# Kernel tuning notes

Hardware: AMD Instinct MI355X
Metric: run time of the kernel (lower is better)

Reference implementation:

```python
import jax, jax.numpy as jnp
import numpy as np

D = 1024      # n_embd
H = 16        # n_head
HD = D // H   # head_size = 64


def _layernorm(x, g, b, eps=1e-5):
    mu = jnp.mean(x, axis=-1, keepdims=True)
    var = jnp.mean((x - mu) ** 2, axis=-1, keepdims=True)
    return (x - mu) * jax.lax.rsqrt(var + eps) * g + b


def setup_inputs() -> dict:
    key = jax.random.key(0)
    ks = jax.random.split(key, 12)
    s = lambda fan_in: 1.0 / np.sqrt(fan_in)
    inp = {
        "x": jax.random.normal(ks[0], (4, 2048, D), dtype=jnp.float32),
        # attention projections (bias=False in Head), per-head weights fused into [D, D]
        "wq": jax.random.uniform(ks[1], (D, D), jnp.float32, -s(D), s(D)),
        "wk": jax.random.uniform(ks[2], (D, D), jnp.float32, -s(D), s(D)),
        "wv": jax.random.uniform(ks[3], (D, D), jnp.float32, -s(D), s(D)),
        "wo": jax.random.uniform(ks[4], (D, D), jnp.float32, -s(D), s(D)),
        "bo": jax.random.uniform(ks[5], (D,), jnp.float32, -s(D), s(D)),
        # feed-forward: D -> 4D -> D
        "w1": jax.random.uniform(ks[6], (D, 4 * D), jnp.float32, -s(D), s(D)),
        "b1": jax.random.uniform(ks[7], (4 * D,), jnp.float32, -s(D), s(D)),
        "w2": jax.random.uniform(ks[8], (4 * D, D), jnp.float32, -s(4 * D), s(4 * D)),
        "b2": jax.random.uniform(ks[9], (D,), jnp.float32, -s(4 * D), s(4 * D)),
        # layernorms
        "g_ln1": jnp.ones((D,), jnp.float32),
        "b_ln1": jnp.zeros((D,), jnp.float32),
        "g_ln2": jnp.ones((D,), jnp.float32),
        "b_ln2": jnp.zeros((D,), jnp.float32),
    }
    return inp


def reference(x, wq, wk, wv, wo, bo, w1, b1, w2, b2, g_ln1, b_ln1, g_ln2, b_ln2):
    B, T, _ = x.shape
    # --- self-attention on ln1(x) ---
    h = _layernorm(x, g_ln1, b_ln1)
    q = (h @ wq).reshape(B, T, H, HD)
    k = (h @ wk).reshape(B, T, H, HD)
    v = (h @ wv).reshape(B, T, H, HD)
    scores = jnp.einsum("bqhd,bkhd->bhqk", q, k) * (HD ** -0.5)
    causal = jnp.tril(jnp.ones((T, T), dtype=bool))
    scores = jnp.where(causal, scores, -jnp.inf)
    wei = jax.nn.softmax(scores, axis=-1)                    # [B,H,T,T]
    attn = jnp.einsum("bhqk,bkhd->bqhd", wei, v).reshape(B, T, D)
    x = x + attn @ wo + bo
    # --- feed-forward on ln2(x) ---
    h2 = _layernorm(x, g_ln2, b_ln2)
    x = x + jax.nn.relu(h2 @ w1 + b1) @ w2 + b2
    return x
```

## Files before the change

kernel.cpp:

```cpp
#include <hip/hip_runtime.h>
#include <cstdint>

typedef __bf16 bf16x8 __attribute__((ext_vector_type(8)));
typedef float f32x4 __attribute__((ext_vector_type(4)));
typedef unsigned int u32x4 __attribute__((ext_vector_type(4)));
typedef unsigned int u32x2 __attribute__((ext_vector_type(2)));
typedef unsigned short u16x4 __attribute__((ext_vector_type(4)));

#define D_MODEL 1024
#define SEQ     2048
#define NBATCH  4
#define NHEAD   16
#define HDIM    64
#define NTOK    (NBATCH * SEQ)
#define QSCALE  0.18033688011112042f

__device__ __forceinline__ unsigned short f2bf(float f) {
  unsigned int u = __builtin_bit_cast(unsigned int, f);
  u += 0x7FFFu + ((u >> 16) & 1u);
  return (unsigned short)(u >> 16);
}

__device__ __forceinline__ float bf2f(unsigned short s) {
  return __builtin_bit_cast(float, (unsigned int)s << 16);
}

__device__ __forceinline__ bf16x8 load8bf(const unsigned short* p) {
  return __builtin_bit_cast(bf16x8, *(const u32x4*)p);
}

__device__ __forceinline__ f32x4 mfma16(bf16x8 a, bf16x8 b, f32x4 c) {
  return __builtin_amdgcn_mfma_f32_16x16x32_bf16(a, b, c, 0, 0, 0);
}

__device__ __forceinline__ void gload16(const unsigned short* g, unsigned short* l) {
  __builtin_amdgcn_global_load_lds((__attribute__((address_space(1))) void*)g,
                                   (__attribute__((address_space(3))) void*)l, 16, 0, 0);
}

__global__ __launch_bounds__(256) void tcast_all(const float* __restrict__ wq,
                                                 const float* __restrict__ wk,
                                                 const float* __restrict__ wv,
                                                 const float* __restrict__ wo,
                                                 const float* __restrict__ w1,
                                                 const float* __restrict__ w2,
                                                 unsigned short* __restrict__ wqkv_t,
                                                 unsigned short* __restrict__ wo_t,
                                                 unsigned short* __restrict__ w1_t,
                                                 unsigned short* __restrict__ w2_t) {
  const int id = blockIdx.x;
  const float* in; unsigned short* out; int K, N, k0, n0;
  if (id < 4096) {
    const int seg = id >> 10, r = id & 1023;
    in  = seg == 0 ? wq : seg == 1 ? wk : seg == 2 ? wv : wo;
    out = seg == 3 ? wo_t : wqkv_t + (size_t)seg * 1024 * 1024;
    K = 1024; N = 1024; n0 = (r & 31) * 32; k0 = (r >> 5) * 32;
  } else if (id < 8192) {
    const int r = id - 4096;
    in = w1; out = w1_t; K = 1024; N = 4096;
    n0 = (r & 127) * 32; k0 = (r >> 7) * 32;
  } else {
    const int r = id - 8192;
    in = w2; out = w2_t; K = 4096; N = 1024;
    n0 = (r & 31) * 32; k0 = (r >> 5) * 32;
  }
  __shared__ float tile[32][33];
  const int tx = threadIdx.x & 31, ty = threadIdx.x >> 5;
  #pragma unroll
  for (int j = 0; j < 4; ++j)
    tile[ty + 8 * j][tx] = in[(size_t)(k0 + ty + 8 * j) * N + n0 + tx];
  __syncthreads();
  #pragma unroll
  for (int j = 0; j < 4; ++j)
    out[(size_t)(n0 + ty + 8 * j) * K + k0 + tx] = f2bf(tile[tx][ty + 8 * j]);
}

template <int FPIN>
__global__ __launch_bounds__(256) void ln_kernel(const void* __restrict__ xin,
                                                 const float* __restrict__ g,
                                                 const float* __restrict__ bb,
                                                 unsigned short* __restrict__ out) {
  const int row = blockIdx.x, tid = threadIdx.x;
  float4 xv;
  if (FPIN) {
    xv = ((const float4*)((const float*)xin + (size_t)row * D_MODEL))[tid];
  } else {
    const u16x4 bv4 = ((const u16x4*)((const unsigned short*)xin + (size_t)row * D_MODEL))[tid];
    xv.x = bf2f(bv4.x); xv.y = bf2f(bv4.y); xv.z = bf2f(bv4.z); xv.w = bf2f(bv4.w);
  }
  float s  = xv.x + xv.y + xv.z + xv.w;
  float ss = xv.x * xv.x + xv.y * xv.y + xv.z * xv.z + xv.w * xv.w;
  #pragma unroll
  for (int off = 1; off < 64; off <<= 1) { s += __shfl_xor(s, off); ss += __shfl_xor(ss, off); }
  __shared__ float red[8];
  const int wave = tid >> 6, lane = tid & 63;
  if (lane == 0) { red[wave] = s; red[4 + wave] = ss; }
  __syncthreads();
  s  = red[0] + red[1] + red[2] + red[3];
  ss = red[4] + red[5] + red[6] + red[7];
  const float mu   = s * (1.0f / D_MODEL);
  const float var  = ss * (1.0f / D_MODEL) - mu * mu;
  const float rstd = rsqrtf(var + 1e-5f);
  const float4 gv = ((const float4*)g)[tid];
  const float4 bv = ((const float4*)bb)[tid];
  u16x4 o;
  o.x = f2bf((xv.x - mu) * rstd * gv.x + bv.x);
  o.y = f2bf((xv.y - mu) * rstd * gv.y + bv.y);
  o.z = f2bf((xv.z - mu) * rstd * gv.z + bv.z);
  o.w = f2bf((xv.w - mu) * rstd * gv.w + bv.w);
  *(u16x4*)(out + (size_t)row * D_MODEL + tid * 4) = o;
}

template <bool BIAS, bool RELU, int RES, bool OBF>
__global__ __launch_bounds__(256) void gemm_bt(const unsigned short* __restrict__ A,
                                               const unsigned short* __restrict__ Bt,
                                               const float* __restrict__ bias,
                                               const void* __restrict__ res,
                                               void* __restrict__ out,
                                               int M, int N, int K) {
  __shared__ __align__(16) unsigned short As[128 * 64];
  __shared__ __align__(16) unsigned short Bs[128 * 64];
  const int tid  = threadIdx.x;
  const int lin = blockIdx.y * gridDim.x + blockIdx.x;
  const int xcd = lin & 7, idx = lin >> 3;
  const int by = xcd * 8 + (idx & 7);
  const int bx = idx >> 3;
  const int row0 = by * 128, col0 = bx * 128;
  const int wave = tid >> 6, lane = tid & 63;
  const int wm = wave >> 1, wn = wave & 1;
  const int l15 = lane & 15, quad = lane >> 4;
  f32x4 acc[4][4] = {};

  const int tr = tid >> 3;
  const int tc = (tid & 7) ^ (tr & 7);
  const unsigned short* gA = A  + (size_t)(row0 + tr) * K + tc * 8;
  const unsigned short* gB = Bt + (size_t)(col0 + tr) * K + tc * 8;

  const int rowA = (wm * 64 + l15) * 64;
  const int rowB = (wn * 64 + l15) * 64;
  const int swz0 = (quad ^ (l15 & 7)) * 8;
  const int swz1 = ((4 + quad) ^ (l15 & 7)) * 8;

  for (int k0 = 0; k0 < K; k0 += 64) {
    #pragma unroll
    for (int i = 0; i < 4; ++i) {
      gload16(gA + (size_t)(i * 32) * K + k0, As + (i * 256 + tid) * 8);
      gload16(gB + (size_t)(i * 32) * K + k0, Bs + (i * 256 + tid) * 8);
    }
    __syncthreads();
    #pragma unroll
    for (int kf = 0; kf < 2; ++kf) {
      const int swz = kf ? swz1 : swz0;
      bf16x8 af[4], bfr[4];
      #pragma unroll
      for (int t = 0; t < 4; ++t) {
        af[t]  = load8bf(As + rowA + t * 1024 + swz);
        bfr[t] = load8bf(Bs + rowB + t * 1024 + swz);
      }
      #pragma unroll
      for (int i = 0; i < 4; ++i)
        #pragma unroll
        for (int j = 0; j < 4; ++j)
          acc[i][j] = mfma16(af[i], bfr[j], acc[i][j]);
    }
    __syncthreads();
  }

  const size_t rbase = (size_t)row0 + wm * 64 + quad * 4;
  const int cbase = col0 + wn * 64 + l15;
  #pragma unroll
  for (int i = 0; i < 4; ++i) {
    #pragma unroll
    for (int j = 0; j < 4; ++j) {
      const int col = cbase + j * 16;
      const float bval = BIAS ? bias[col] : 0.0f;
      #pragma unroll
      for (int r = 0; r < 4; ++r) {
        const size_t row = rbase + i * 16 + r;
        float v = acc[i][j][r];
        if (BIAS) v += bval;
        if (RELU) v = fmaxf(v, 0.0f);
        if (RES == 1) v += ((const float*)res)[row * N + col];
        if (RES == 2) v += bf2f(((const unsigned short*)res)[row * N + col]);
        if (OBF)  ((unsigned short*)out)[row * N + col] = f2bf(v);
        else      ((float*)out)[row * N + col] = v;
      }
    }
  }
}

__device__ __forceinline__ void stage_half_512(const unsigned short* __restrict__ src,
                                               unsigned short* dst, int ld, int k0,
                                               int h, int tid) {
  #pragma unroll
  for (int l = 0; l < 2; ++l) {
    const int cid = l * 512 + tid;
    const int r = cid >> 3, p = cid & 7, c = p ^ (r & 7);
    gload16(src + (size_t)(h * 128 + r) * ld + k0 + c * 8, dst + h * 8192 + cid * 8);
  }
}

template <bool BIAS, bool RELU, int RES, bool OBF, bool QKV>
__global__ __launch_bounds__(512, 2) void gemm256(const unsigned short* __restrict__ A,
                                                  const unsigned short* __restrict__ Bt,
                                                  const float* __restrict__ bias,
                                                  const void* __restrict__ res,
                                                  void* __restrict__ out,
                                                  unsigned short* __restrict__ qb,
                                                  unsigned short* __restrict__ kp,
                                                  unsigned short* __restrict__ vt,
                                                  int M, int N, int K) {
  __shared__ __align__(16) unsigned short lds[2][32768];
  const int tid = threadIdx.x;
  const int lin = blockIdx.y * gridDim.x + blockIdx.x;
  const int xcd = lin & 7, idx = lin >> 3;
  const int by = xcd * 4 + (idx & 3);
  const int bx = idx >> 2;
  const int row0 = by * 256, col0 = bx * 256;
  const int wave = tid >> 6, lane = tid & 63;
  const int wm = wave >> 2, wn = wave & 3;
  const int l15 = lane & 15, quad = lane >> 4;
  const int swz0 = (quad ^ (l15 & 7)) * 8;
  const int swz1 = ((4 + quad) ^ (l15 & 7)) * 8;

  const unsigned short* gA = A  + (size_t)row0 * K;
  const unsigned short* gB = Bt + (size_t)col0 * K;

  unsigned short* As0 = &lds[0][0];
  unsigned short* Bs0 = &lds[0][16384];
  unsigned short* As1 = &lds[1][0];
  unsigned short* Bs1 = &lds[1][16384];

  f32x4 acc[8][4] = {};
  const int KT = K >> 6;

  stage_half_512(gA, As0, K, 0, 0, tid);
  stage_half_512(gA, As0, K, 0, 1, tid);
  stage_half_512(gB, Bs0, K, 0, 0, tid);
  stage_half_512(gB, Bs0, K, 0, 1, tid);
  if (KT > 1) {
    stage_half_512(gB, Bs1, K, 64, 0, tid);
    stage_half_512(gB, Bs1, K, 64, 1, tid);
    asm volatile("s_waitcnt vmcnt(4)" ::: "memory");
  } else {
    asm volatile("s_waitcnt vmcnt(0)" ::: "memory");
  }
  asm volatile("s_barrier" ::: "memory");

  for (int t = 0; t < KT; ++t) {
    unsigned short* As  = (t & 1) ? As1 : As0;
    unsigned short* Bs  = (t & 1) ? Bs1 : Bs0;
    unsigned short* Asn = (t & 1) ? As0 : As1;
    const int k1 = (t + 1) << 6, k2 = (t + 2) << 6;
    bf16x8 a0[2][4], b01[2][2], b23[2][2];

    #pragma unroll
    for (int i = 0; i < 4; ++i) {
      const unsigned short* ap = As + (wm * 128 + i * 16 + l15) * 64;
      a0[0][i] = load8bf(ap + swz0);
      a0[1][i] = load8bf(ap + swz1);
    }
    #pragma unroll
    for (int j = 0; j < 2; ++j) {
      const unsigned short* bp = Bs + (wn * 64 + j * 16 + l15) * 64;
      b01[0][j] = load8bf(bp + swz0);
      b01[1][j] = load8bf(bp + swz1);
      const unsigned short* bp2 = Bs + (wn * 64 + 32 + j * 16 + l15) * 64;
      b23[0][j] = load8bf(bp2 + swz0);
      b23[1][j] = load8bf(bp2 + swz1);
    }
    if (t + 1 < KT) {
      stage_half_512(gA, Asn, K, k1, 0, tid);
      stage_half_512(gA, Asn, K, k1, 1, tid);
    }
    __builtin_amdgcn_s_setprio(1);
    #pragma unroll
    for (int kf = 0; kf < 2; ++kf)
      #pragma unroll
      for (int i = 0; i < 4; ++i)
        #pragma unroll
        for (int j = 0; j < 2; ++j)
          acc[i][j] = mfma16(a0[kf][i], b01[kf][j], acc[i][j]);
    #pragma unroll
    for (int kf = 0; kf < 2; ++kf)
      #pragma unroll
      for (int i = 0; i < 4; ++i)
        #pragma unroll
        for (int j = 0; j < 2; ++j)
          acc[i][2 + j] = mfma16(a0[kf][i], b23[kf][j], acc[i][2 + j]);
    __builtin_amdgcn_s_setprio(0);
    __builtin_amdgcn_sched_barrier(0);
    asm volatile("s_barrier" ::: "memory");

    #pragma unroll
    for (int i = 0; i < 4; ++i) {
      const unsigned short* ap = As + (wm * 128 + 64 + i * 16 + l15) * 64;
      a0[0][i] = load8bf(ap + swz0);
      a0[1][i] = load8bf(ap + swz1);
    }
    if (t + 2 < KT) {
      stage_half_512(gB, Bs, K, k2, 0, tid);
      stage_half_512(gB, Bs, K, k2, 1, tid);
    }
    __builtin_amdgcn_s_setprio(1);
    #pragma unroll
    for (int kf = 0; kf < 2; ++kf)
      #pragma unroll
      for (int i = 0; i < 4; ++i)
        #pragma unroll
        for (int j = 0; j < 2; ++j)
          acc[4 + i][2 + j] = mfma16(a0[kf][i], b23[kf][j], acc[4 + i][2 + j]);
    #pragma unroll
    for (int kf = 0; kf < 2; ++kf)
      #pragma unroll
      for (int i = 0; i < 4; ++i)
        #pragma unroll
        for (int j = 0; j < 2; ++j)
          acc[4 + i][j] = mfma16(a0[kf][i], b01[kf][j], acc[4 + i][j]);
    __builtin_amdgcn_s_setprio(0);
    __builtin_amdgcn_sched_barrier(0);
    if (t + 2 < KT) asm volatile("s_waitcnt vmcnt(4)" ::: "memory");
    else            asm volatile("s_waitcnt vmcnt(0)" ::: "memory");
    asm volatile("s_barrier" ::: "memory");
  }

  const size_t rbase = (size_t)row0 + wm * 128 + quad * 4;
  const int cbase = col0 + wn * 64 + l15;
  if (QKV) {
    const int sec = col0 >> 10;
    #pragma unroll
    for (int i = 0; i < 8; ++i) {
      #pragma unroll
      for (int j = 0; j < 4; ++j) {
        const int col = cbase + j * 16;
        if (sec == 0) {
          #pragma unroll
          for (int r = 0; r < 4; ++r) {
            const size_t row = rbase + i * 16 + r;
            qb[row * 1024 + col] = f2bf(acc[i][j][r] * QSCALE);
          }
        } else if (sec == 1) {
          const int c2 = col - 1024, hh = c2 >> 6, d = c2 & 63;
          #pragma unroll
          for (int r = 0; r < 4; ++r) {
            const size_t row = rbase + i * 16 + r;
            const int bb = (int)(row >> 11), tt = (int)(row & 2047);
            kp[(((size_t)(bb * 16 + hh)) * SEQ + tt) * 64 + d] = f2bf(acc[i][j][r]);
          }
        } else {
          const int c2 = col - 2048, hh = c2 >> 6, d = c2 & 63;
          const size_t t0 = rbase + i * 16;
          const int bb = (int)(t0 >> 11);
          u16x4 pk;
          #pragma unroll
          for (int r = 0; r < 4; ++r) pk[r] = f2bf(acc[i][j][r]);
          *(u16x4*)(vt + ((size_t)(bb * 16 + hh) * 64 + d) * SEQ + (t0 & 2047)) = pk;
        }
      }
    }
  } else {
    #pragma unroll
    for (int i = 0; i < 8; ++i) {
      #pragma unroll
      for (int j = 0; j < 4; ++j) {
        const int col = cbase + j * 16;
        const float bval = BIAS ? bias[col] : 0.0f;
        #pragma unroll
        for (int r = 0; r < 4; ++r) {
          const size_t row = rbase + i * 16 + r;
          float v = acc[i][j][r];
          if (BIAS) v += bval;
          if (RELU) v = fmaxf(v, 0.0f);
          if (RES == 1) v += ((const float*)res)[row * N + col];
          if (RES == 2) v += bf2f(((const unsigned short*)res)[row * N + col]);
          if (OBF)  ((unsigned short*)out)[row * N + col] = f2bf(v);
          else      ((float*)out)[row * N + col] = v;
        }
      }
    }
  }
  (void)M;
}

__device__ __forceinline__ void stage32g(const unsigned short* __restrict__ src,
                                         unsigned short* dst, int ld, int k0,
                                         int h128, int t256) {
  #pragma unroll
  for (int l = 0; l < 2; ++l) {
    const int cid = l * 256 + t256;
    const int L = cid >> 3;
    const int p = cid & 7;
    const int c = p ^ (L & 7);
    const int row = h128 * 128 + L * 2 + (c >> 2);
    gload16(src + (size_t)row * ld + k0 + (c & 3) * 8, dst + h128 * 4096 + cid * 8);
  }
}

__device__ __forceinline__ bf16x8 frag32(const unsigned short* tile, int r0,
                                         int l15, int quad) {
  const int row = r0 + l15;
  const int L = row >> 1;
  const int p = ((row & 1) * 4 + quad) ^ (L & 7);
  return load8bf(tile + L * 64 + p * 8);
}

__global__ __launch_bounds__(512, 2) void gemm_ffn2(const unsigned short* __restrict__ A,
                                                    const unsigned short* __restrict__ Bt,
                                                    const float* __restrict__ bias,
                                                    const unsigned short* __restrict__ res,
                                                    float* __restrict__ out) {
  __shared__ __align__(16) unsigned short lds[2][2][12288];
  const int tid = threadIdx.x;
  const int lin = blockIdx.y * gridDim.x + blockIdx.x;
  const int xcd = lin & 7, idx = lin >> 3;
  const int by = xcd * 4 + (idx & 3);
  const int bx = idx >> 2;
  const int row0 = by * 256, col0 = bx * 128;
  const int wave = tid >> 6, lane = tid & 63;
  const int ks = wave >> 2;
  const int w4 = wave & 3;
  const int wm = w4 >> 1, wn = w4 & 1;
  const int l15 = lane & 15, quad = lane >> 4;
  const int t256 = tid & 255;

  const unsigned short* gA = A  + (size_t)row0 * 4096 + ks * 2048;
  const unsigned short* gB = Bt + (size_t)col0 * 4096 + ks * 2048;

  unsigned short* As0 = &lds[ks][0][0];
  unsigned short* Bs0 = &lds[ks][0][8192];
  unsigned short* As1 = &lds[ks][1][0];
  unsigned short* Bs1 = &lds[ks][1][8192];

  f32x4 acc[8][4] = {};
  const int KT = 64;

  stage32g(gA, As0, 4096, 0, 0, t256);
  stage32g(gA, As0, 4096, 0, 1, t256);
  stage32g(gB, Bs0, 4096, 0, 0, t256);
  stage32g(gB, Bs1, 4096, 32, 0, t256);
  asm volatile("s_waitcnt vmcnt(2)" ::: "memory");
  asm volatile("s_barrier" ::: "memory");

  for (int t = 0; t < KT; ++t) {
    unsigned short* As  = (t & 1) ? As1 : As0;
    unsigned short* Bs  = (t & 1) ? Bs1 : Bs0;
    unsigned short* Asn = (t & 1) ? As0 : As1;
    const int k1 = (t + 1) << 5, k2 = (t + 2) << 5;
    bf16x8 a[4], b[4];

    #pragma unroll
    for (int j = 0; j < 4; ++j) b[j] = frag32(Bs, wn * 64 + j * 16, l15, quad);
    #pragma unroll
    for (int i = 0; i < 4; ++i) a[i] = frag32(As, wm * 128 + i * 16, l15, quad);
    if (t + 1 < KT) {
      stage32g(gA, Asn, 4096, k1, 0, t256);
      stage32g(gA, Asn, 4096, k1, 1, t256);
    }
    __builtin_amdgcn_s_setprio(1);
    #pragma unroll
    for (int i = 0; i < 4; ++i)
      #pragma unroll
      for (int j = 0; j < 4; ++j)
        acc[i][j] = mfma16(a[i], b[j], acc[i][j]);
    __builtin_amdgcn_s_setprio(0);
    __builtin_amdgcn_sched_barrier(0);
    asm volatile("s_barrier" ::: "memory");

    #pragma unroll
    for (int i = 0; i < 4; ++i) a[i] = frag32(As, wm * 128 + 64 + i * 16, l15, quad);
    if (t + 2 < KT) stage32g(gB, Bs, 4096, k2, 0, t256);
    __builtin_amdgcn_s_setprio(1);
    #pragma unroll
    for (int i = 0; i < 4; ++i)
      #pragma unroll
      for (int j = 0; j < 4; ++j)
        acc[4 + i][j] = mfma16(a[i], b[j], acc[4 + i][j]);
    __builtin_amdgcn_s_setprio(0);
    __builtin_amdgcn_sched_barrier(0);
    if (t + 2 < KT) asm volatile("s_waitcnt vmcnt(2)" ::: "memory");
    else            asm volatile("s_waitcnt vmcnt(0)" ::: "memory");
    asm volatile("s_barrier" ::: "memory");
  }

  float* ex = (float*)&lds[0][0][0];
  #pragma unroll
  for (int half = 0; half < 2; ++half) {
    __syncthreads();
    if (ks == 1) {
      #pragma unroll
      for (int i = 0; i < 4; ++i)
        #pragma unroll
        for (int j = 0; j < 4; ++j)
          *(f32x4*)(ex + ((size_t)(w4 * 16 + i * 4 + j)) * 256 + lane * 4) =
              acc[half * 4 + i][j];
    }
    __syncthreads();
    if (ks == 0) {
      #pragma unroll
      for (int i = 0; i < 4; ++i)
        #pragma unroll
        for (int j = 0; j < 4; ++j) {
          const f32x4 v = *(const f32x4*)(ex + ((size_t)(w4 * 16 + i * 4 + j)) * 256 + lane * 4);
          acc[half * 4 + i][j] += v;
        }
    }
  }
  if (ks == 0) {
    const size_t rbase = (size_t)row0 + wm * 128 + quad * 4;
    const int cbase = col0 + wn * 64 + l15;
    #pragma unroll
    for (int i = 0; i < 8; ++i) {
      #pragma unroll
      for (int j = 0; j < 4; ++j) {
        const int col = cbase + j * 16;
        const float bval = bias[col];
        #pragma unroll
        for (int r = 0; r < 4; ++r) {
          const size_t row = rbase + i * 16 + r;
          out[row * 1024 + col] = acc[i][j][r] + bval + bf2f(res[row * 1024 + col]);
        }
      }
    }
  }
}

__global__ __launch_bounds__(256) void attn5(const unsigned short* __restrict__ qb,
                                             const unsigned short* __restrict__ kp,
                                             const unsigned short* __restrict__ vt,
                                             unsigned short* __restrict__ attnb) {
  const int lin = (blockIdx.z * 16 + blockIdx.y) * 8 + blockIdx.x;
  const int xcd = lin & 7, idx = lin >> 3;
  const int bh = xcd * 8 + (idx >> 3);
  const int xb = idx & 7;
  const int b = bh >> 4, h = bh & 15;
  const int tid = threadIdx.x, wave = tid >> 6, lane = tid & 63;
  const int l15 = lane & 15, quad = lane >> 4;
  const size_t tokbase = (size_t)b * SEQ;

  __shared__ __align__(16) unsigned short ks[2][64 * 64];
  __shared__ __align__(16) unsigned short vts[2][64 * 64];
  __shared__ __align__(16) unsigned short plds[4][32 * 64];

  const unsigned short* kbase = kp + (size_t)bh * SEQ * HDIM;
  const unsigned short* vbase = vt + (size_t)bh * HDIM * SEQ;

  for (int half = 0; half < 2; ++half) {
    const int qblk = (half == 0) ? (15 - xb) : xb;
    const int qw0 = qblk * 128 + wave * 32;

    bf16x8 qf[2][2];
    #pragma unroll
    for (int qfi = 0; qfi < 2; ++qfi)
      #pragma unroll
      for (int kf = 0; kf < 2; ++kf)
        qf[qfi][kf] = load8bf(qb + (tokbase + qw0 + qfi * 16 + l15) * 1024
                              + h * HDIM + kf * 32 + quad * 8);

    f32x4 o[2][4] = {};
    float lsum[2] = {0.0f, 0.0f};

    const int ntiles = qblk * 2 + 2;

    {
      #pragma unroll
      for (int i = 0; i < 2; ++i) {
        const int cid = i * 256 + tid;
        const int r = cid >> 3, p = cid & 7, c = p ^ (r & 7);
        gload16(kbase + (size_t)r * HDIM + c * 8, &ks[0][cid * 8]);
      }
      #pragma unroll
      for (int i = 0; i < 2; ++i) {
        const int cid = i * 256 + tid;
        const int d = cid >> 3, p = cid & 7, c = p ^ (d & 7);
        gload16(vbase + (size_t)d * SEQ + c * 8, &vts[0][cid * 8]);
      }
      asm volatile("s_waitcnt vmcnt(0)" ::: "memory");
      asm volatile("s_barrier" ::: "memory");
    }

    for (int kt = 0; kt < ntiles; ++kt) {
      const int k0 = kt * 64;
      if (kt + 1 < ntiles) {
        const int kn = (kt + 1) * 64;
        const int nb = (kt + 1) & 1;
        #pragma unroll
        for (int i = 0; i < 2; ++i) {
          const int cid = i * 256 + tid;
          const int r = cid >> 3, p = cid & 7, c = p ^ (r & 7);
          gload16(kbase + (size_t)(kn + r) * HDIM + c * 8, &ks[nb][cid * 8]);
        }
        #pragma unroll
        for (int i = 0; i < 2; ++i) {
          const int cid = i * 256 + tid;
          const int d = cid >> 3, p = cid & 7, c = p ^ (d & 7);
          gload16(vbase + (size_t)d * SEQ + kn + c * 8, &vts[nb][cid * 8]);
        }
      }
      if (k0 <= qw0 + 31) {
        const unsigned short* ksb  = ks[kt & 1];
        const unsigned short* vtsb = vts[kt & 1];
        f32x4 s[4][2] = {};
        #pragma unroll
        for (int kf = 0; kf < 2; ++kf)
          #pragma unroll
          for (int keyf = 0; keyf < 4; ++keyf) {
            const int row = keyf * 16 + l15;
            const int p = (kf * 4 + quad) ^ (row & 7);
            const bf16x8 kfr = load8bf(ksb + row * 64 + p * 8);
            s[keyf][0] = mfma16(kfr, qf[0][kf], s[keyf][0]);
            s[keyf][1] = mfma16(kfr, qf[1][kf], s[keyf][1]);
          }
        #pragma unroll
        for (int qfi = 0; qfi < 2; ++qfi) {
          const int q = qw0 + qfi * 16 + l15;
          const int qloc = qfi * 16 + l15;
          #pragma unroll
          for (int keyf = 0; keyf < 4; ++keyf) {
            unsigned int pw[4];
            #pragma unroll
            for (int r = 0; r < 4; ++r) {
              const int key = k0 + keyf * 16 + quad * 4 + r;
              float p = __builtin_amdgcn_exp2f(s[keyf][qfi][r]);
              p = (key > q) ? 0.0f : p;
              pw[r] = __builtin_bit_cast(unsigned int, p);
              lsum[qfi] += __builtin_bit_cast(float, pw[r] & 0xFFFF0000u);
            }
            u32x2 packed;
            packed.x = (pw[0] >> 16) | (pw[1] & 0xFFFF0000u);
            packed.y = (pw[2] >> 16) | (pw[3] & 0xFFFF0000u);
            const int slot = (keyf * 4 + quad) ^ ((l15 & 7) << 1);
            *(u32x2*)(&plds[wave][qloc * 64 + slot * 4]) = packed;
          }
        }
        asm volatile("s_waitcnt lgkmcnt(0)" ::: "memory");
        __builtin_amdgcn_sched_barrier(0);
        #pragma unroll
        for (int kf = 0; kf < 2; ++kf) {
          bf16x8 pa[2];
          #pragma unroll
          for (int mf = 0; mf < 2; ++mf) {
            const int lq = mf * 16 + l15;
            const int c = (kf * 4 + quad) ^ (l15 & 7);
            pa[mf] = load8bf(&plds[wave][lq * 64 + c * 8]);
          }
          #pragma unroll
          for (int df = 0; df < 4; ++df) {
            const int row = df * 16 + l15;
            const int p = (kf * 4 + quad) ^ (row & 7);
            const bf16x8 vb = load8bf(vtsb + row * 64 + p * 8);
            o[0][df] = mfma16(pa[0], vb, o[0][df]);
            o[1][df] = mfma16(pa[1], vb, o[1][df]);
          }
        }
      }
      __builtin_amdgcn_sched_barrier(0);
      asm volatile("s_waitcnt vmcnt(0)" ::: "memory");
      asm volatile("s_barrier" ::: "memory");
    }
    #pragma unroll
    for (int mf = 0; mf < 2; ++mf) {
      float l = lsum[mf];
      l += __shfl_xor(l, 16);
      l += __shfl_xor(l, 32);
      const float rl = 1.0f / l;
      #pragma unroll
      for (int r = 0; r < 4; ++r) {
        const float rv = __shfl(rl, quad * 4 + r);
        const size_t row = tokbase + qw0 + mf * 16 + quad * 4 + r;
        #pragma unroll
        for (int df = 0; df < 4; ++df)
          attnb[row * D_MODEL + h * HDIM + df * 16 + l15] = f2bf(o[mf][df][r] * rv);
      }
    }
  }
}

extern "C" void kernel_launch(void* const* d_in, const int* in_sizes, int n_in,
                              void* d_out, int out_size, void* d_ws, size_t ws_size,
                              hipStream_t stream) {
  const float* x    = (const float*)d_in[0];
  const float* wq   = (const float*)d_in[1];
  const float* wk   = (const float*)d_in[2];
  const float* wv   = (const float*)d_in[3];
  const float* wo   = (const float*)d_in[4];
  const float* bo   = (const float*)d_in[5];
  const float* w1   = (const float*)d_in[6];
  const float* b1   = (const float*)d_in[7];
  const float* w2   = (const float*)d_in[8];
  const float* b2   = (const float*)d_in[9];
  const float* g1   = (const float*)d_in[10];
  const float* bl1  = (const float*)d_in[11];
  const float* g2   = (const float*)d_in[12];
  const float* bl2  = (const float*)d_in[13];
  float* out = (float*)d_out;

  char* ws = (char*)d_ws;
  size_t off = 0;
  auto alloc = [&](size_t bytes) { char* p = ws + off; off += (bytes + 255) & ~(size_t)255; return p; };
  unsigned short* wqkv_t = (unsigned short*)alloc((size_t)3072 * 1024 * 2);
  unsigned short* wo_t   = (unsigned short*)alloc((size_t)1024 * 1024 * 2);
  unsigned short* w1_t   = (unsigned short*)alloc((size_t)4096 * 1024 * 2);
  unsigned short* w2_t   = (unsigned short*)alloc((size_t)1024 * 4096 * 2);
  unsigned short* h1     = (unsigned short*)alloc((size_t)NTOK * 1024 * 2);
  unsigned short* kpb    = (unsigned short*)alloc((size_t)NTOK * 1024 * 2);
  unsigned short* vtb    = (unsigned short*)alloc((size_t)NTOK * 1024 * 2);
  unsigned short* attnb  = (unsigned short*)alloc((size_t)NTOK * 1024 * 2);
  unsigned short* h2     = (unsigned short*)alloc((size_t)NTOK * 1024 * 2);
  unsigned short* ffn1   = (unsigned short*)alloc((size_t)NTOK * 4096 * 2);
  unsigned short* qb  = attnb;
  unsigned short* x1b = h1;

  tcast_all<<<12288, 256, 0, stream>>>(wq, wk, wv, wo, w1, w2,
                                       wqkv_t, wo_t, w1_t, w2_t);
  ln_kernel<1><<<NTOK, 256, 0, stream>>>(x, g1, bl1, h1);
  gemm256<false, false, 0, true, true><<<dim3(12, 32), 512, 0, stream>>>(
      h1, wqkv_t, nullptr, nullptr, nullptr, qb, kpb, vtb, NTOK, 3072, 1024);
  attn5<<<dim3(SEQ / 256, NHEAD, NBATCH), 256, 0, stream>>>(qb, kpb, vtb, attnb);
  gemm_bt<true, false, 1, true><<<dim3(8, 64), 256, 0, stream>>>(
      attnb, wo_t, bo, x, x1b, NTOK, 1024, 1024);
  ln_kernel<0><<<NTOK, 256, 0, stream>>>(x1b, g2, bl2, h2);
  gemm256<true, true, 0, true, false><<<dim3(16, 32), 512, 0, stream>>>(
      h2, w1_t, b1, nullptr, ffn1, nullptr, nullptr, nullptr, NTOK, 4096, 1024);
  gemm_ffn2<<<dim3(8, 32), 512, 0, stream>>>(ffn1, w2_t, b2, x1b, out);
  (void)in_sizes; (void)n_in; (void)out_size; (void)ws_size;
}
```

Measured before the change: 445.6 us.

## Generalize split-K 256x128 GEMM and use it for QKV and output projections

Turns the FFN2 split-K kernel, which splits K across two wave groups and reduces through LDS, into a templated gemm_sk with bias, relu, residual and QKV scatter epilogues. The QKV projection moves to it from the 256x256 gemm256, using twice as many workgroups. The Wo projection moves to it from the simple 128x128 gemm_bt, gaining pipelined double-buffered loads. The cost is the extra LDS reduction and smaller N tiles, which means more A re-reads.

```diff
diff --git a/kernel.cpp b/kernel.cpp
--- a/kernel.cpp
+++ b/kernel.cpp
@@ -111,84 +111,6 @@
   *(u16x4*)(out + (size_t)row * D_MODEL + tid * 4) = o;
 }
 
-template <bool BIAS, bool RELU, int RES, bool OBF>
-__global__ __launch_bounds__(256) void gemm_bt(const unsigned short* __restrict__ A,
-                                               const unsigned short* __restrict__ Bt,
-                                               const float* __restrict__ bias,
-                                               const void* __restrict__ res,
-                                               void* __restrict__ out,
-                                               int M, int N, int K) {
-  __shared__ __align__(16) unsigned short As[128 * 64];
-  __shared__ __align__(16) unsigned short Bs[128 * 64];
-  const int tid  = threadIdx.x;
-  const int lin = blockIdx.y * gridDim.x + blockIdx.x;
-  const int xcd = lin & 7, idx = lin >> 3;
-  const int by = xcd * 8 + (idx & 7);
-  const int bx = idx >> 3;
-  const int row0 = by * 128, col0 = bx * 128;
-  const int wave = tid >> 6, lane = tid & 63;
-  const int wm = wave >> 1, wn = wave & 1;
-  const int l15 = lane & 15, quad = lane >> 4;
-  f32x4 acc[4][4] = {};
-
-  const int tr = tid >> 3;
-  const int tc = (tid & 7) ^ (tr & 7);
-  const unsigned short* gA = A  + (size_t)(row0 + tr) * K + tc * 8;
-  const unsigned short* gB = Bt + (size_t)(col0 + tr) * K + tc * 8;
-
-  const int rowA = (wm * 64 + l15) * 64;
-  const int rowB = (wn * 64 + l15) * 64;
-  const int swz0 = (quad ^ (l15 & 7)) * 8;
-  const int swz1 = ((4 + quad) ^ (l15 & 7)) * 8;
-
-  for (int k0 = 0; k0 < K; k0 += 64) {
-    #pragma unroll
-    for (int i = 0; i < 4; ++i) {
-      gload16(gA + (size_t)(i * 32) * K + k0, As + (i * 256 + tid) * 8);
-      gload16(gB + (size_t)(i * 32) * K + k0, Bs + (i * 256 + tid) * 8);
-    }
-    __syncthreads();
-    #pragma unroll
-    for (int kf = 0; kf < 2; ++kf) {
-      const int swz = kf ? swz1 : swz0;
-      bf16x8 af[4], bfr[4];
-      #pragma unroll
-      for (int t = 0; t < 4; ++t) {
-        af[t]  = load8bf(As + rowA + t * 1024 + swz);
-        bfr[t] = load8bf(Bs + rowB + t * 1024 + swz);
-      }
-      #pragma unroll
-      for (int i = 0; i < 4; ++i)
-        #pragma unroll
-        for (int j = 0; j < 4; ++j)
-          acc[i][j] = mfma16(af[i], bfr[j], acc[i][j]);
-    }
-    __syncthreads();
-  }
-
-  const size_t rbase = (size_t)row0 + wm * 64 + quad * 4;
-  const int cbase = col0 + wn * 64 + l15;
-  #pragma unroll
-  for (int i = 0; i < 4; ++i) {
-    #pragma unroll
-    for (int j = 0; j < 4; ++j) {
-      const int col = cbase + j * 16;
-      const float bval = BIAS ? bias[col] : 0.0f;
-      #pragma unroll
-      for (int r = 0; r < 4; ++r) {
-        const size_t row = rbase + i * 16 + r;
-        float v = acc[i][j][r];
-        if (BIAS) v += bval;
-        if (RELU) v = fmaxf(v, 0.0f);
-        if (RES == 1) v += ((const float*)res)[row * N + col];
-        if (RES == 2) v += bf2f(((const unsigned short*)res)[row * N + col]);
-        if (OBF)  ((unsigned short*)out)[row * N + col] = f2bf(v);
-        else      ((float*)out)[row * N + col] = v;
-      }
-    }
-  }
-}
-
 __device__ __forceinline__ void stage_half_512(const unsigned short* __restrict__ src,
                                                unsigned short* dst, int ld, int k0,
                                                int h, int tid) {
@@ -200,15 +122,12 @@
   }
 }
 
-template <bool BIAS, bool RELU, int RES, bool OBF, bool QKV>
+template <bool BIAS, bool RELU, int RES, bool OBF>
 __global__ __launch_bounds__(512, 2) void gemm256(const unsigned short* __restrict__ A,
                                                   const unsigned short* __restrict__ Bt,
                                                   const float* __restrict__ bias,
                                                   const void* __restrict__ res,
                                                   void* __restrict__ out,
-                                                  unsigned short* __restrict__ qb,
-                                                  unsigned short* __restrict__ kp,
-                                                  unsigned short* __restrict__ vt,
                                                   int M, int N, int K) {
   __shared__ __align__(16) unsigned short lds[2][32768];
   const int tid = threadIdx.x;
@@ -323,6 +242,161 @@
     else            asm volatile("s_waitcnt vmcnt(0)" ::: "memory");
     asm volatile("s_barrier" ::: "memory");
   }
+
+  const size_t rbase = (size_t)row0 + wm * 128 + quad * 4;
+  const int cbase = col0 + wn * 64 + l15;
+  #pragma unroll
+  for (int i = 0; i < 8; ++i) {
+    #pragma unroll
+    for (int j = 0; j < 4; ++j) {
+      const int col = cbase + j * 16;
+      const float bval = BIAS ? bias[col] : 0.0f;
+      #pragma unroll
+      for (int r = 0; r < 4; ++r) {
+        const size_t row = rbase + i * 16 + r;
+        float v = acc[i][j][r];
+        if (BIAS) v += bval;
+        if (RELU) v = fmaxf(v, 0.0f);
+        if (RES == 1) v += ((const float*)res)[row * N + col];
+        if (RES == 2) v += bf2f(((const unsigned short*)res)[row * N + col]);
+        if (OBF)  ((unsigned short*)out)[row * N + col] = f2bf(v);
+        else      ((float*)out)[row * N + col] = v;
+      }
+    }
+  }
+  (void)M;
+}
+
+__device__ __forceinline__ void stage32g(const unsigned short* __restrict__ src,
+                                         unsigned short* dst, int ld, int k0,
+                                         int h128, int t256) {
+  #pragma unroll
+  for (int l = 0; l < 2; ++l) {
+    const int cid = l * 256 + t256;
+    const int L = cid >> 3;
+    const int p = cid & 7;
+    const int c = p ^ (L & 7);
+    const int row = h128 * 128 + L * 2 + (c >> 2);
+    gload16(src + (size_t)row * ld + k0 + (c & 3) * 8, dst + h128 * 4096 + cid * 8);
+  }
+}
+
+__device__ __forceinline__ bf16x8 frag32(const unsigned short* tile, int r0,
+                                         int l15, int quad) {
+  const int row = r0 + l15;
+  const int L = row >> 1;
+  const int p = ((row & 1) * 4 + quad) ^ (L & 7);
+  return load8bf(tile + L * 64 + p * 8);
+}
+
+template <bool BIAS, bool RELU, int RES, bool OBF, bool QKV>
+__global__ __launch_bounds__(512, 2) void gemm_sk(const unsigned short* __restrict__ A,
+                                                  const unsigned short* __restrict__ Bt,
+                                                  const float* __restrict__ bias,
+                                                  const void* __restrict__ res,
+                                                  void* __restrict__ out,
+                                                  unsigned short* __restrict__ qb,
+                                                  unsigned short* __restrict__ kp,
+                                                  unsigned short* __restrict__ vt,
+                                                  int Ktot) {
+  __shared__ __align__(16) unsigned short lds[2][2][12288];
+  const int tid = threadIdx.x;
+  const int lin = blockIdx.y * gridDim.x + blockIdx.x;
+  const int xcd = lin & 7, idx = lin >> 3;
+  const int by = xcd * 4 + (idx & 3);
+  const int bx = idx >> 2;
+  const int row0 = by * 256, col0 = bx * 128;
+  const int wave = tid >> 6, lane = tid & 63;
+  const int ks = wave >> 2;
+  const int w4 = wave & 3;
+  const int wm = w4 >> 1, wn = w4 & 1;
+  const int l15 = lane & 15, quad = lane >> 4;
+  const int t256 = tid & 255;
+
+  const int kh = Ktot >> 1;
+  const unsigned short* gA = A  + (size_t)row0 * Ktot + ks * kh;
+  const unsigned short* gB = Bt + (size_t)col0 * Ktot + ks * kh;
+
+  unsigned short* As0 = &lds[ks][0][0];
+  unsigned short* Bs0 = &lds[ks][0][8192];
+  unsigned short* As1 = &lds[ks][1][0];
+  unsigned short* Bs1 = &lds[ks][1][8192];
+
+  f32x4 acc[8][4] = {};
+  const int KT = kh >> 5;
+
+  stage32g(gA, As0, Ktot, 0, 0, t256);
+  stage32g(gA, As0, Ktot, 0, 1, t256);
+  stage32g(gB, Bs0, Ktot, 0, 0, t256);
+  stage32g(gB, Bs1, Ktot, 32, 0, t256);
+  asm volatile("s_waitcnt vmcnt(2)" ::: "memory");
+  asm volatile("s_barrier" ::: "memory");
+
+  for (int t = 0; t < KT; ++t) {
+    unsigned short* As  = (t & 1) ? As1 : As0;
+    unsigned short* Bs  = (t & 1) ? Bs1 : Bs0;
+    unsigned short* Asn = (t & 1) ? As0 : As1;
+    const int k1 = (t + 1) << 5, k2 = (t + 2) << 5;
+    bf16x8 a[4], b[4];
+
+    #pragma unroll
+    for (int j = 0; j < 4; ++j) b[j] = frag32(Bs, wn * 64 + j * 16, l15, quad);
+    #pragma unroll
+    for (int i = 0; i < 4; ++i) a[i] = frag32(As, wm * 128 + i * 16, l15, quad);
+    if (t + 1 < KT) {
+      stage32g(gA, Asn, Ktot, k1, 0, t256);
+      stage32g(gA, Asn, Ktot, k1, 1, t256);
+    }
+    __builtin_amdgcn_s_setprio(1);
+    #pragma unroll
+    for (int i = 0; i < 4; ++i)
+      #pragma unroll
+      for (int j = 0; j < 4; ++j)
+        acc[i][j] = mfma16(a[i], b[j], acc[i][j]);
+    __builtin_amdgcn_s_setprio(0);
+    __builtin_amdgcn_sched_barrier(0);
+    asm volatile("s_barrier" ::: "memory");
+
+    #pragma unroll
+    for (int i = 0; i < 4; ++i) a[i] = frag32(As, wm * 128 + 64 + i * 16, l15, quad);
+    if (t + 2 < KT) stage32g(gB, Bs, Ktot, k2, 0, t256);
+    __builtin_amdgcn_s_setprio(1);
+    #pragma unroll
+    for (int i = 0; i < 4; ++i)
+      #pragma unroll
+      for (int j = 0; j < 4; ++j)
+        acc[4 + i][j] = mfma16(a[i], b[j], acc[4 + i][j]);
+    __builtin_amdgcn_s_setprio(0);
+    __builtin_amdgcn_sched_barrier(0);
+    if (t + 2 < KT) asm volatile("s_waitcnt vmcnt(2)" ::: "memory");
+    else            asm volatile("s_waitcnt vmcnt(0)" ::: "memory");
+    asm volatile("s_barrier" ::: "memory");
+  }
+
+  float* ex = (float*)&lds[0][0][0];
+  #pragma unroll
+  for (int half = 0; half < 2; ++half) {
+    __syncthreads();
+    if (ks == 1) {
+      #pragma unroll
+      for (int i = 0; i < 4; ++i)
+        #pragma unroll
+        for (int j = 0; j < 4; ++j)
+          *(f32x4*)(ex + ((size_t)(w4 * 16 + i * 4 + j)) * 256 + lane * 4) =
+              acc[half * 4 + i][j];
+    }
+    __syncthreads();
+    if (ks == 0) {
+      #pragma unroll
+      for (int i = 0; i < 4; ++i)
+        #pragma unroll
+        for (int j = 0; j < 4; ++j) {
+          const f32x4 v = *(const f32x4*)(ex + ((size_t)(w4 * 16 + i * 4 + j)) * 256 + lane * 4);
+          acc[half * 4 + i][j] += v;
+        }
+    }
+  }
+  if (ks != 0) return;
 
   const size_t rbase = (size_t)row0 + wm * 128 + quad * 4;
   const int cbase = col0 + wn * 64 + l15;
@@ -371,153 +445,10 @@
           float v = acc[i][j][r];
           if (BIAS) v += bval;
           if (RELU) v = fmaxf(v, 0.0f);
-          if (RES == 1) v += ((const float*)res)[row * N + col];
-          if (RES == 2) v += bf2f(((const unsigned short*)res)[row * N + col]);
-          if (OBF)  ((unsigned short*)out)[row * N + col] = f2bf(v);
-          else      ((float*)out)[row * N + col] = v;
-        }
-      }
-    }
-  }
-  (void)M;
-}
-
-__device__ __forceinline__ void stage32g(const unsigned short* __restrict__ src,
-                                         unsigned short* dst, int ld, int k0,
-                                         int h128, int t256) {
-  #pragma unroll
-  for (int l = 0; l < 2; ++l) {
-    const int cid = l * 256 + t256;
-    const int L = cid >> 3;
-    const int p = cid & 7;
-    const int c = p ^ (L & 7);
-    const int row = h128 * 128 + L * 2 + (c >> 2);
-    gload16(src + (size_t)row * ld + k0 + (c & 3) * 8, dst + h128 * 4096 + cid * 8);
-  }
-}
-
-__device__ __forceinline__ bf16x8 frag32(const unsigned short* tile, int r0,
-                                         int l15, int quad) {
-  const int row = r0 + l15;
-  const int L = row >> 1;
-  const int p = ((row & 1) * 4 + quad) ^ (L & 7);
-  return load8bf(tile + L * 64 + p * 8);
-}
-
-__global__ __launch_bounds__(512, 2) void gemm_ffn2(const unsigned short* __restrict__ A,
-                                                    const unsigned short* __restrict__ Bt,
-                                                    const float* __restrict__ bias,
-                                                    const unsigned short* __restrict__ res,
-                                                    float* __restrict__ out) {
-  __shared__ __align__(16) unsigned short lds[2][2][12288];
-  const int tid = threadIdx.x;
-  const int lin = blockIdx.y * gridDim.x + blockIdx.x;
-  const int xcd = lin & 7, idx = lin >> 3;
-  const int by = xcd * 4 + (idx & 3);
-  const int bx = idx >> 2;
-  const int row0 = by * 256, col0 = bx * 128;
-  const int wave = tid >> 6, lane = tid & 63;
-  const int ks = wave >> 2;
-  const int w4 = wave & 3;
-  const int wm = w4 >> 1, wn = w4 & 1;
-  const int l15 = lane & 15, quad = lane >> 4;
-  const int t256 = tid & 255;
-
-  const unsigned short* gA = A  + (size_t)row0 * 4096 + ks * 2048;
-  const unsigned short* gB = Bt + (size_t)col0 * 4096 + ks * 2048;
-
-  unsigned short* As0 = &lds[ks][0][0];
-  unsigned short* Bs0 = &lds[ks][0][8192];
-  unsigned short* As1 = &lds[ks][1][0];
-  unsigned short* Bs1 = &lds[ks][1][8192];
-
-  f32x4 acc[8][4] = {};
-  const int KT = 64;
-
-  stage32g(gA, As0, 4096, 0, 0, t256);
-  stage32g(gA, As0, 4096, 0, 1, t256);
-  stage32g(gB, Bs0, 4096, 0, 0, t256);
-  stage32g(gB, Bs1, 4096, 32, 0, t256);
-  asm volatile("s_waitcnt vmcnt(2)" ::: "memory");
-  asm volatile("s_barrier" ::: "memory");
-
-  for (int t = 0; t < KT; ++t) {
-    unsigned short* As  = (t & 1) ? As1 : As0;
-    unsigned short* Bs  = (t & 1) ? Bs1 : Bs0;
-    unsigned short* Asn = (t & 1) ? As0 : As1;
-    const int k1 = (t + 1) << 5, k2 = (t + 2) << 5;
-    bf16x8 a[4], b[4];
-
-    #pragma unroll
-    for (int j = 0; j < 4; ++j) b[j] = frag32(Bs, wn * 64 + j * 16, l15, quad);
-    #pragma unroll
-    for (int i = 0; i < 4; ++i) a[i] = frag32(As, wm * 128 + i * 16, l15, quad);
-    if (t + 1 < KT) {
-      stage32g(gA, Asn, 4096, k1, 0, t256);
-      stage32g(gA, Asn, 4096, k1, 1, t256);
-    }
-    __builtin_amdgcn_s_setprio(1);
-    #pragma unroll
-    for (int i = 0; i < 4; ++i)
-      #pragma unroll
-      for (int j = 0; j < 4; ++j)
-        acc[i][j] = mfma16(a[i], b[j], acc[i][j]);
-    __builtin_amdgcn_s_setprio(0);
-    __builtin_amdgcn_sched_barrier(0);
-    asm volatile("s_barrier" ::: "memory");
-
-    #pragma unroll
-    for (int i = 0; i < 4; ++i) a[i] = frag32(As, wm * 128 + 64 + i * 16, l15, quad);
-    if (t + 2 < KT) stage32g(gB, Bs, 4096, k2, 0, t256);
-    __builtin_amdgcn_s_setprio(1);
-    #pragma unroll
-    for (int i = 0; i < 4; ++i)
-      #pragma unroll
-      for (int j = 0; j < 4; ++j)
-        acc[4 + i][j] = mfma16(a[i], b[j], acc[4 + i][j]);
-    __builtin_amdgcn_s_setprio(0);
-    __builtin_amdgcn_sched_barrier(0);
-    if (t + 2 < KT) asm volatile("s_waitcnt vmcnt(2)" ::: "memory");
-    else            asm volatile("s_waitcnt vmcnt(0)" ::: "memory");
-    asm volatile("s_barrier" ::: "memory");
-  }
-
-  float* ex = (float*)&lds[0][0][0];
-  #pragma unroll
-  for (int half = 0; half < 2; ++half) {
-    __syncthreads();
-    if (ks == 1) {
-      #pragma unroll
-      for (int i = 0; i < 4; ++i)
-        #pragma unroll
-        for (int j = 0; j < 4; ++j)
-          *(f32x4*)(ex + ((size_t)(w4 * 16 + i * 4 + j)) * 256 + lane * 4) =
-              acc[half * 4 + i][j];
-    }
-    __syncthreads();
-    if (ks == 0) {
-      #pragma unroll
-      for (int i = 0; i < 4; ++i)
-        #pragma unroll
-        for (int j = 0; j < 4; ++j) {
-          const f32x4 v = *(const f32x4*)(ex + ((size_t)(w4 * 16 + i * 4 + j)) * 256 + lane * 4);
-          acc[half * 4 + i][j] += v;
-        }
-    }
-  }
-  if (ks == 0) {
-    const size_t rbase = (size_t)row0 + wm * 128 + quad * 4;
-    const int cbase = col0 + wn * 64 + l15;
-    #pragma unroll
-    for (int i = 0; i < 8; ++i) {
-      #pragma unroll
-      for (int j = 0; j < 4; ++j) {
-        const int col = cbase + j * 16;
-        const float bval = bias[col];
-        #pragma unroll
-        for (int r = 0; r < 4; ++r) {
-          const size_t row = rbase + i * 16 + r;
-          out[row * 1024 + col] = acc[i][j][r] + bval + bf2f(res[row * 1024 + col]);
+          if (RES == 1) v += ((const float*)res)[row * 1024 + col];
+          if (RES == 2) v += bf2f(((const unsigned short*)res)[row * 1024 + col]);
+          if (OBF)  ((unsigned short*)out)[row * 1024 + col] = f2bf(v);
+          else      ((float*)out)[row * 1024 + col] = v;
         }
       }
     }
@@ -713,14 +644,15 @@
   tcast_all<<<12288, 256, 0, stream>>>(wq, wk, wv, wo, w1, w2,
                                        wqkv_t, wo_t, w1_t, w2_t);
   ln_kernel<1><<<NTOK, 256, 0, stream>>>(x, g1, bl1, h1);
-  gemm256<false, false, 0, true, true><<<dim3(12, 32), 512, 0, stream>>>(
-      h1, wqkv_t, nullptr, nullptr, nullptr, qb, kpb, vtb, NTOK, 3072, 1024);
+  gemm_sk<false, false, 0, true, true><<<dim3(24, 32), 512, 0, stream>>>(
+      h1, wqkv_t, nullptr, nullptr, nullptr, qb, kpb, vtb, 1024);
   attn5<<<dim3(SEQ / 256, NHEAD, NBATCH), 256, 0, stream>>>(qb, kpb, vtb, attnb);
-  gemm_bt<true, false, 1, true><<<dim3(8, 64), 256, 0, stream>>>(
-      attnb, wo_t, bo, x, x1b, NTOK, 1024, 1024);
+  gemm_sk<true, false, 1, true, false><<<dim3(8, 32), 512, 0, stream>>>(
+      attnb, wo_t, bo, x, x1b, nullptr, nullptr, nullptr, 1024);
   ln_kernel<0><<<NTOK, 256, 0, stream>>>(x1b, g2, bl2, h2);
-  gemm256<true, true, 0, true, false><<<dim3(16, 32), 512, 0, stream>>>(
-      h2, w1_t, b1, nullptr, ffn1, nullptr, nullptr, nullptr, NTOK, 4096, 1024);
-  gemm_ffn2<<<dim3(8, 32), 512, 0, stream>>>(ffn1, w2_t, b2, x1b, out);
+  gemm256<true, true, 0, true><<<dim3(16, 32), 512, 0, stream>>>(
+      h2, w1_t, b1, nullptr, ffn1, NTOK, 4096, 1024);
+  gemm_sk<true, false, 2, false, false><<<dim3(8, 32), 512, 0, stream>>>(
+      ffn1, w2_t, b2, x1b, out, nullptr, nullptr, nullptr, 4096);
   (void)in_sizes; (void)n_in; (void)out_size; (void)ws_size;
 }
```

New measurement: 465.8 us. 4.5% more time.
